# Kernel optimization log

Hardware: AMD Instinct MI355X
Metric: run time of the kernel (lower is better)

The kernel has to match this reference:

```python
import jax, jax.numpy as jnp
import numpy as np

# dims: N sentences, L tokens each, M=2 memory slots/sentence, D hidden, H heads
N, L, M, D, H, FF, V, P, LAYERS = 4, 256, 2, 768, 12, 3072, 32000, 1024, 4
DH = D // H


def setup_inputs() -> dict:
    key = jax.random.key(0)
    ks = jax.random.split(key, 20)
    s = 0.02
    inp = {
        'input_ids': jax.random.randint(ks[0], (N, L), 0, V),
        'memory': jax.random.normal(ks[1], (N, M, D), jnp.float32),
        'emb_table': jax.random.normal(ks[2], (V, D), jnp.float32) * s,
        'pos_table': jax.random.normal(ks[3], (P + 2, D), jnp.float32) * s,
        'Wq': jax.random.normal(ks[4], (LAYERS, D, D), jnp.float32) * s,
        'bq': jnp.zeros((LAYERS, D), jnp.float32),
        'Wk': jax.random.normal(ks[5], (LAYERS, D, D), jnp.float32) * s,
        'bk': jnp.zeros((LAYERS, D), jnp.float32),
        'Wv': jax.random.normal(ks[6], (LAYERS, D, D), jnp.float32) * s,
        'bv': jnp.zeros((LAYERS, D), jnp.float32),
        'W1': jax.random.normal(ks[7], (LAYERS, D, FF), jnp.float32) * s,
        'b1': jnp.zeros((LAYERS, FF), jnp.float32),
        'W2': jax.random.normal(ks[8], (LAYERS, FF, D), jnp.float32) * s,
        'b2': jnp.zeros((LAYERS, D), jnp.float32),
        'g1': jnp.ones((LAYERS, D), jnp.float32),
        'be1': jnp.zeros((LAYERS, D), jnp.float32),
        'g2': jnp.ones((LAYERS, D), jnp.float32),
        'be2': jnp.zeros((LAYERS, D), jnp.float32),
    }
    return inp


def _layer_norm(x, g, b):
    mu = jnp.mean(x, axis=-1, keepdims=True)
    var = jnp.mean((x - mu) ** 2, axis=-1, keepdims=True)
    return (x - mu) / jnp.sqrt(var + 1e-5) * g + b


def _encoder(input_ids, memory, emb_table, pos_table, Wq, bq, Wk, bk, Wv, bv,
             W1, b1, W2, b2, g1, be1, g2, be2):
    base = N * M            # token rows start here in the packed input
    T = base + N * L        # total rows (memory rows + token rows)
    Kk = M + L              # keys per query (own memory + own tokens)

    # position embeddings: memory rows get pos (p % M); tokens get id_pos + M
    mem_pos = jnp.tile(jnp.arange(M), N)                    # (N*M,)
    mem = memory.reshape(N * M, D) + pos_table[mem_pos]
    fwd_pos = jnp.tile(jnp.arange(L) + M, N)                # (N*L,)
    tok = emb_table[input_ids.reshape(-1)] + pos_table[fwd_pos]
    x = jnp.concatenate([mem, tok], axis=0)                 # (T, D)

    # per-sentence key set: its M memory rows then its L token rows
    key_pos = jnp.concatenate([
        jnp.arange(N)[:, None] * M + jnp.arange(M)[None, :],
        base + jnp.arange(N)[:, None] * L + jnp.arange(L)[None, :],
    ], axis=1)                                              # (N, Kk)
    sent = jnp.concatenate([jnp.repeat(jnp.arange(N), M),
                            jnp.repeat(jnp.arange(N), L)])  # (T,)
    gidx = key_pos[sent]                                    # (T, Kk)
    # equal-length sentences => the additive mask built by the torch code is
    # all zeros (key_len == max_key_len for every row), so it is omitted.

    scale = 1.0 / np.sqrt(DH)
    for i in range(LAYERS):
        # K/V are linear row-wise, so project once on all rows then gather
        # (identical math to projecting the gathered tgt, without T-fold GEMM)
        q = (x @ Wq[i] + bq[i]).reshape(T, H, DH)
        kf = (x @ Wk[i] + bk[i]).reshape(T, H, DH)
        vf = (x @ Wv[i] + bv[i]).reshape(T, H, DH)
        kg = kf[gidx]                                       # (T, Kk, H, DH)
        vg = vf[gidx]
        scores = jnp.einsum('thd,tkhd->thk', q, kg) * scale
        probs = jax.nn.softmax(scores, axis=-1)
        ctx = jnp.einsum('thk,tkhd->thd', probs, vg).reshape(T, D)
        x = _layer_norm(x + ctx, g1[i], be1[i])
        h = jax.nn.gelu(x @ W1[i] + b1[i], approximate=False)
        x = _layer_norm(x + h @ W2[i] + b2[i], g2[i], be2[i])

    ret = key_pos[:, M:]                                    # (N, L) token rows
    return x[ret]                                           # (N, L, D)


def reference(input_ids, memory, emb_table, pos_table, Wq, bq, Wk, bk, Wv, bv,
              W1, b1, W2, b2, g1, be1, g2, be2):
    return _encoder(input_ids, memory, emb_table, pos_table, Wq, bq, Wk, bk,
                    Wv, bv, W1, b1, W2, b2, g1, be1, g2, be2)
```

## Files before the change

### kernel.cpp

```cpp
#include <hip/hip_runtime.h>
#include <hip/hip_bf16.h>
#include <math.h>

#define N_      4
#define L_      256
#define M_      2
#define D_      768
#define H_      12
#define FF_     3072
#define DH_     64
#define LAYERS_ 4
#define BASE_   8
#define T_      1032
#define TP_     1088
#define KK_     258
#define QS_     2304
#define PS_     264

typedef __bf16 bf16x8 __attribute__((ext_vector_type(8)));
typedef float  f32x4  __attribute__((ext_vector_type(4)));

__device__ __forceinline__ void async_load16(const __hip_bfloat16* g, __hip_bfloat16* l) {
  __builtin_amdgcn_global_load_lds(
      (const __attribute__((address_space(1))) unsigned int*)g,
      (__attribute__((address_space(3))) unsigned int*)l, 16, 0, 0);
}

__global__ __launch_bounds__(256) void transpose_cast_kernel(
    const float* __restrict__ src, __hip_bfloat16* __restrict__ dst, int K, int N) {
  __shared__ float tile[32][33];
  const int k0 = blockIdx.y * 32, n0 = blockIdx.x * 32;
  const int r = threadIdx.x >> 5, c = threadIdx.x & 31;
  #pragma unroll
  for (int i = 0; i < 4; ++i)
    tile[r + i * 8][c] = src[(size_t)(k0 + r + i * 8) * N + n0 + c];
  __syncthreads();
  #pragma unroll
  for (int i = 0; i < 4; ++i)
    dst[(size_t)(n0 + r + i * 8) * K + k0 + c] = __float2bfloat16(tile[c][r + i * 8]);
}

__global__ __launch_bounds__(256) void pack_bias_kernel(
    const float* __restrict__ bq, const float* __restrict__ bk,
    const float* __restrict__ bv, float* __restrict__ out) {
  int i = blockIdx.x * 256 + threadIdx.x;
  int l = i / QS_, j = i - l * QS_;
  float v;
  if (j < D_)            v = bq[l * D_ + j];
  else if (j < 2 * D_)   v = bk[l * D_ + (j - D_)];
  else                   v = bv[l * D_ + (j - 2 * D_)];
  out[i] = v;
}

__global__ __launch_bounds__(256) void embed_kernel(
    const int* __restrict__ ids, const float* __restrict__ memory,
    const float* __restrict__ emb, const float* __restrict__ pos,
    float* __restrict__ x, __hip_bfloat16* __restrict__ xb) {
  int row = blockIdx.x;
  const float *src, *p;
  if (row < BASE_) {
    src = memory + (long long)row * D_;
    p   = pos + (row & 1) * D_;
  } else {
    int i = row - BASE_;
    int tok = ids[i];
    src = emb + (long long)tok * D_;
    p   = pos + (M_ + (i & (L_ - 1))) * D_;
  }
  for (int d = threadIdx.x; d < D_; d += 256) {
    float v = src[d] + p[d];
    x[(long long)row * D_ + d]  = v;
    xb[(long long)row * D_ + d] = __float2bfloat16(v);
  }
}

template <int ACT, int WF32, int WBF16, int WVT>
__global__ __launch_bounds__(256) void gemm_mfma(
    const __hip_bfloat16* __restrict__ A,
    const __hip_bfloat16* __restrict__ Bt,
    const float* __restrict__ bias,
    float* __restrict__ C,
    __hip_bfloat16* __restrict__ Cb,
    __hip_bfloat16* __restrict__ vt,
    int N, int K) {
  __shared__ __align__(16) __hip_bfloat16 As[4][64][32];
  __shared__ __align__(16) __hip_bfloat16 Bs[4][64][32];
  const int tid  = threadIdx.x;
  const int lane = tid & 63, wid = tid >> 6;
  const int ln   = lane & 15, qd = lane >> 4;
  const int wm   = wid >> 1, wn = wid & 1;

  const size_t arow = (size_t)(blockIdx.y * 64 + wid * 16 + (lane >> 2)) * K + (lane & 3) * 8;
  const size_t brow = (size_t)(blockIdx.x * 64 + wid * 16 + (lane >> 2)) * K + (lane & 3) * 8;

  f32x4 acc[2][2] = {};
  for (int k0 = 0; k0 < K; k0 += 128) {
    #pragma unroll
    for (int s = 0; s < 4; ++s) {
      async_load16(A  + arow + k0 + s * 32, &As[s][wid * 16][0]);
      async_load16(Bt + brow + k0 + s * 32, &Bs[s][wid * 16][0]);
    }
    __syncthreads();
    #pragma unroll
    for (int s = 0; s < 4; ++s) {
      bf16x8 a0 = *(const bf16x8*)&As[s][wm * 32 + ln][qd * 8];
      bf16x8 a1 = *(const bf16x8*)&As[s][wm * 32 + 16 + ln][qd * 8];
      bf16x8 b0 = *(const bf16x8*)&Bs[s][wn * 32 + ln][qd * 8];
      bf16x8 b1 = *(const bf16x8*)&Bs[s][wn * 32 + 16 + ln][qd * 8];
      acc[0][0] = __builtin_amdgcn_mfma_f32_16x16x32_bf16(a0, b0, acc[0][0], 0, 0, 0);
      acc[0][1] = __builtin_amdgcn_mfma_f32_16x16x32_bf16(a0, b1, acc[0][1], 0, 0, 0);
      acc[1][0] = __builtin_amdgcn_mfma_f32_16x16x32_bf16(a1, b0, acc[1][0], 0, 0, 0);
      acc[1][1] = __builtin_amdgcn_mfma_f32_16x16x32_bf16(a1, b1, acc[1][1], 0, 0, 0);
    }
    __syncthreads();
  }
  #pragma unroll
  for (int mt = 0; mt < 2; ++mt) {
    #pragma unroll
    for (int nt = 0; nt < 2; ++nt) {
      const int col = blockIdx.x * 64 + wn * 32 + nt * 16 + ln;
      const float bv = bias[col];
      #pragma unroll
      for (int i = 0; i < 4; ++i) {
        const int row = blockIdx.y * 64 + wm * 32 + mt * 16 + qd * 4 + i;
        float v = acc[mt][nt][i] + bv;
        if (ACT) v = 0.5f * v * (1.f + erff(v * 0.70710678118654752f));
        if (WF32)  C[(size_t)row * N + col]  = v;
        if (WVT) {
          if (col < 2 * D_) Cb[(size_t)row * N + col] = __float2bfloat16(v);
          else              vt[(size_t)(col - 2 * D_) * TP_ + row] = __float2bfloat16(v);
        } else if (WBF16) {
          Cb[(size_t)row * N + col] = __float2bfloat16(v);
        }
      }
    }
  }
}

__global__ __launch_bounds__(256) void attn_mfma(
    const __hip_bfloat16* __restrict__ qkv,
    const __hip_bfloat16* __restrict__ vtb,
    float* __restrict__ ctx) {
  __shared__ __align__(16) __hip_bfloat16 Ps[64][PS_];
  const int qt = blockIdx.x, h = blockIdx.y, b = blockIdx.z;
  const int tid = threadIdx.x;
  const int w = tid >> 6, lane = tid & 63, ln = lane & 15, qd = lane >> 4;

  bf16x8 aq0, aq1;
  {
    int j = qt * 64 + w * 16 + ln;
    int tok = (j < 256) ? (BASE_ + b * L_ + j)
            : ((j < KK_) ? (b * M_ + (j - 256)) : (b * M_));
    const __hip_bfloat16* qp = qkv + (size_t)tok * QS_ + h * DH_ + qd * 8;
    aq0 = *(const bf16x8*)qp;
    aq1 = *(const bf16x8*)(qp + 32);
  }

  f32x4 sa[17];
  #pragma unroll
  for (int nt = 0; nt < 17; ++nt) sa[nt] = (f32x4){0.f, 0.f, 0.f, 0.f};
  #pragma unroll
  for (int nt = 0; nt < 17; ++nt) {
    int key = nt * 16 + ln;
    int ktok = (key < 256) ? (BASE_ + b * L_ + key)
             : ((key < KK_) ? (b * M_ + (key - 256)) : (b * M_));
    const __hip_bfloat16* kp = qkv + (size_t)ktok * QS_ + D_ + h * DH_ + qd * 8;
    bf16x8 b0 = *(const bf16x8*)kp;
    bf16x8 b1 = *(const bf16x8*)(kp + 32);
    sa[nt] = __builtin_amdgcn_mfma_f32_16x16x32_bf16(aq0, b0, sa[nt], 0, 0, 0);
    sa[nt] = __builtin_amdgcn_mfma_f32_16x16x32_bf16(aq1, b1, sa[nt], 0, 0, 0);
  }

  #pragma unroll
  for (int i = 0; i < 4; ++i) {
    float v[17];
    #pragma unroll
    for (int nt = 0; nt < 17; ++nt) v[nt] = sa[nt][i] * 0.125f;
    float mx = -1e30f;
    #pragma unroll
    for (int nt = 0; nt < 16; ++nt) mx = fmaxf(mx, v[nt]);
    if (ln < 2) mx = fmaxf(mx, v[16]);
    #pragma unroll
    for (int m = 1; m < 16; m <<= 1) mx = fmaxf(mx, __shfl_xor(mx, m));
    float sum = 0.f;
    #pragma unroll
    for (int nt = 0; nt < 17; ++nt) {
      float e = (nt == 16 && ln >= 2) ? 0.f : __expf(v[nt] - mx);
      v[nt] = e;
      sum += e;
    }
    #pragma unroll
    for (int m = 1; m < 16; m <<= 1) sum += __shfl_xor(sum, m);
    float is = 1.f / sum;
    const int row = w * 16 + qd * 4 + i;
    #pragma unroll
    for (int nt = 0; nt < 17; ++nt)
      if (nt < 16 || ln < 2)
        Ps[row][nt * 16 + ln] = __float2bfloat16(v[nt] * is);
  }

  f32x4 oa[4] = {};
  #pragma unroll
  for (int k0 = 0; k0 < 8; ++k0) {
    bf16x8 ap = *(const bf16x8*)&Ps[w * 16 + ln][k0 * 32 + qd * 8];
    #pragma unroll
    for (int nt = 0; nt < 4; ++nt) {
      const __hip_bfloat16* vp = vtb + (size_t)(h * DH_ + nt * 16 + ln) * TP_
                               + BASE_ + b * L_ + k0 * 32 + qd * 8;
      bf16x8 bv = *(const bf16x8*)vp;
      oa[nt] = __builtin_amdgcn_mfma_f32_16x16x32_bf16(ap, bv, oa[nt], 0, 0, 0);
    }
  }
  {
    float p0[4], p1[4];
    #pragma unroll
    for (int i = 0; i < 4; ++i) {
      p0[i] = __bfloat162float(Ps[w * 16 + qd * 4 + i][256]);
      p1[i] = __bfloat162float(Ps[w * 16 + qd * 4 + i][257]);
    }
    #pragma unroll
    for (int nt = 0; nt < 4; ++nt) {
      const __hip_bfloat16* vp = vtb + (size_t)(h * DH_ + nt * 16 + ln) * TP_ + b * M_;
      float v0 = __bfloat162float(vp[0]);
      float v1 = __bfloat162float(vp[1]);
      #pragma unroll
      for (int i = 0; i < 4; ++i) oa[nt][i] += p0[i] * v0 + p1[i] * v1;
    }
  }

  #pragma unroll
  for (int i = 0; i < 4; ++i) {
    int j = qt * 64 + w * 16 + qd * 4 + i;
    if (j < KK_) {
      int tok = (j < 256) ? (BASE_ + b * L_ + j) : (b * M_ + (j - 256));
      #pragma unroll
      for (int nt = 0; nt < 4; ++nt)
        ctx[(size_t)tok * D_ + h * DH_ + nt * 16 + ln] = oa[nt][i];
    }
  }
}

__global__ __launch_bounds__(256) void add_ln_kernel(
    float* __restrict__ x, const float* __restrict__ delta,
    const float* __restrict__ g, const float* __restrict__ b,
    __hip_bfloat16* __restrict__ xb) {
  __shared__ float sred[4];
  __shared__ float sbc;
  const int t = blockIdx.x, tid = threadIdx.x;
  float y[3];
  float s = 0.f;
  #pragma unroll
  for (int i = 0; i < 3; ++i) {
    int d = tid + i * 256;
    y[i] = x[(long long)t * D_ + d] + delta[(long long)t * D_ + d];
    s += y[i];
  }
  #pragma unroll
  for (int o = 32; o > 0; o >>= 1) s += __shfl_down(s, o);
  if ((tid & 63) == 0) sred[tid >> 6] = s;
  __syncthreads();
  if (tid == 0) sbc = (sred[0] + sred[1] + sred[2] + sred[3]) * (1.f / D_);
  __syncthreads();
  const float mu = sbc;
  __syncthreads();
  float vs = 0.f;
  #pragma unroll
  for (int i = 0; i < 3; ++i) { float d = y[i] - mu; vs += d * d; }
  #pragma unroll
  for (int o = 32; o > 0; o >>= 1) vs += __shfl_down(vs, o);
  if ((tid & 63) == 0) sred[tid >> 6] = vs;
  __syncthreads();
  if (tid == 0) sbc = (sred[0] + sred[1] + sred[2] + sred[3]) * (1.f / D_);
  __syncthreads();
  const float inv = rsqrtf(sbc + 1e-5f);
  #pragma unroll
  for (int i = 0; i < 3; ++i) {
    int d = tid + i * 256;
    float v = (y[i] - mu) * inv * g[d] + b[d];
    x[(long long)t * D_ + d]  = v;
    xb[(long long)t * D_ + d] = __float2bfloat16(v);
  }
}

__global__ __launch_bounds__(256) void out_copy_kernel(
    const float* __restrict__ x, float* __restrict__ out, int n) {
  int i = blockIdx.x * 256 + threadIdx.x;
  if (i < n) out[i] = x[BASE_ * D_ + i];
}

extern "C" void kernel_launch(void* const* d_in, const int* in_sizes, int n_in,
                              void* d_out, int out_size, void* d_ws, size_t ws_size,
                              hipStream_t stream) {
  const int*   ids    = (const int*)  d_in[0];
  const float* memory = (const float*)d_in[1];
  const float* emb    = (const float*)d_in[2];
  const float* pos    = (const float*)d_in[3];
  const float* Wq     = (const float*)d_in[4];
  const float* bq     = (const float*)d_in[5];
  const float* Wk     = (const float*)d_in[6];
  const float* bk     = (const float*)d_in[7];
  const float* Wv     = (const float*)d_in[8];
  const float* bv     = (const float*)d_in[9];
  const float* W1     = (const float*)d_in[10];
  const float* b1     = (const float*)d_in[11];
  const float* W2     = (const float*)d_in[12];
  const float* b2     = (const float*)d_in[13];
  const float* g1     = (const float*)d_in[14];
  const float* be1    = (const float*)d_in[15];
  const float* g2     = (const float*)d_in[16];
  const float* be2    = (const float*)d_in[17];

  char* w = (char*)d_ws;
  float* x    = (float*)w;                      w += (size_t)TP_ * D_ * 4;
  float* cb   = (float*)w;                      w += (size_t)TP_ * D_ * 4;
  float* bqkv = (float*)w;                      w += (size_t)LAYERS_ * QS_ * 4;
  __hip_bfloat16* xb    = (__hip_bfloat16*)w;   w += (size_t)TP_ * D_ * 2;
  __hip_bfloat16* qkvb  = (__hip_bfloat16*)w;   w += (size_t)TP_ * QS_ * 2;
  __hip_bfloat16* vtb   = (__hip_bfloat16*)w;   w += (size_t)D_ * TP_ * 2;
  __hip_bfloat16* hbb   = (__hip_bfloat16*)w;   w += (size_t)TP_ * FF_ * 2;
  __hip_bfloat16* Wqkvt = (__hip_bfloat16*)w;   w += (size_t)LAYERS_ * QS_ * D_ * 2;
  __hip_bfloat16* W1t   = (__hip_bfloat16*)w;   w += (size_t)LAYERS_ * FF_ * D_ * 2;
  __hip_bfloat16* W2t   = (__hip_bfloat16*)w;   w += (size_t)LAYERS_ * D_ * FF_ * 2;

  for (int i = 0; i < LAYERS_; ++i) {
    const size_t wo  = (size_t)i * D_ * D_;
    const size_t wo1 = (size_t)i * D_ * FF_;
    __hip_bfloat16* dqkv = Wqkvt + (size_t)i * QS_ * D_;
    transpose_cast_kernel<<<dim3(D_ / 32, D_ / 32), 256, 0, stream>>>(Wq + wo, dqkv,                       D_, D_);
    transpose_cast_kernel<<<dim3(D_ / 32, D_ / 32), 256, 0, stream>>>(Wk + wo, dqkv + (size_t)D_ * D_,     D_, D_);
    transpose_cast_kernel<<<dim3(D_ / 32, D_ / 32), 256, 0, stream>>>(Wv + wo, dqkv + (size_t)2 * D_ * D_, D_, D_);
    transpose_cast_kernel<<<dim3(FF_ / 32, D_ / 32), 256, 0, stream>>>(W1 + wo1, W1t + (size_t)i * FF_ * D_, D_, FF_);
    transpose_cast_kernel<<<dim3(D_ / 32, FF_ / 32), 256, 0, stream>>>(W2 + wo1, W2t + (size_t)i * D_ * FF_, FF_, D_);
  }
  pack_bias_kernel<<<LAYERS_ * QS_ / 256, 256, 0, stream>>>(bq, bk, bv, bqkv);

  embed_kernel<<<T_, 256, 0, stream>>>(ids, memory, emb, pos, x, xb);

  for (int i = 0; i < LAYERS_; ++i) {
    gemm_mfma<0, 0, 1, 1><<<dim3(QS_ / 64, TP_ / 64), 256, 0, stream>>>(
        xb, Wqkvt + (size_t)i * QS_ * D_, bqkv + i * QS_, nullptr, qkvb, vtb, QS_, D_);
    attn_mfma<<<dim3(5, H_, N_), 256, 0, stream>>>(qkvb, vtb, cb);
    add_ln_kernel<<<T_, 256, 0, stream>>>(x, cb, g1 + i * D_, be1 + i * D_, xb);
    gemm_mfma<1, 0, 1, 0><<<dim3(FF_ / 64, TP_ / 64), 256, 0, stream>>>(
        xb, W1t + (size_t)i * FF_ * D_, b1 + i * FF_, nullptr, hbb, nullptr, FF_, D_);
    gemm_mfma<0, 1, 0, 0><<<dim3(D_ / 64, TP_ / 64), 256, 0, stream>>>(
        hbb, W2t + (size_t)i * D_ * FF_, b2 + i * D_, cb, nullptr, nullptr, D_, FF_);
    add_ln_kernel<<<T_, 256, 0, stream>>>(x, cb, g2 + i * D_, be2 + i * D_, xb);
  }

  out_copy_kernel<<<(out_size + 255) / 256, 256, 0, stream>>>(x, (float*)d_out, out_size);
}
```

Baseline: 601.2 us.

## Use 128x128 MFMA tiles for QKV/FFN1 GEMMs and batch weight-prep kernels

```diff
diff --git a/kernel.cpp b/kernel.cpp
--- a/kernel.cpp
+++ b/kernel.cpp
@@ -12,7 +12,7 @@
 #define LAYERS_ 4
 #define BASE_   8
 #define T_      1032
-#define TP_     1088
+#define TP_     1152
 #define KK_     258
 #define QS_     2304
 #define PS_     264
@@ -26,7 +26,7 @@
       (__attribute__((address_space(3))) unsigned int*)l, 16, 0, 0);
 }
 
-__global__ __launch_bounds__(256) void transpose_cast_kernel(
+__device__ __forceinline__ void tile_transpose(
     const float* __restrict__ src, __hip_bfloat16* __restrict__ dst, int K, int N) {
   __shared__ float tile[32][33];
   const int k0 = blockIdx.y * 32, n0 = blockIdx.x * 32;
@@ -36,8 +36,35 @@
     tile[r + i * 8][c] = src[(size_t)(k0 + r + i * 8) * N + n0 + c];
   __syncthreads();
   #pragma unroll
-  for (int i = 0; i < 4; ++i)
-    dst[(size_t)(n0 + r + i * 8) * K + k0 + c] = __float2bfloat16(tile[c][r + i * 8]);
+  for (int i = 0; i < 2; ++i) {
+    int e = threadIdx.x + i * 256;
+    int n = e >> 4, kp = e & 15;
+    __hip_bfloat162 v;
+    v.x = __float2bfloat16(tile[2 * kp][n]);
+    v.y = __float2bfloat16(tile[2 * kp + 1][n]);
+    *(__hip_bfloat162*)&dst[(size_t)(n0 + n) * K + k0 + 2 * kp] = v;
+  }
+}
+
+__global__ __launch_bounds__(256) void prep_qkv_kernel(
+    const float* __restrict__ Wq, const float* __restrict__ Wk,
+    const float* __restrict__ Wv, __hip_bfloat16* __restrict__ Wqkvt) {
+  const int z = blockIdx.z, layer = z / 3, which = z - layer * 3;
+  const float* src = (which == 0 ? Wq : which == 1 ? Wk : Wv) + (size_t)layer * D_ * D_;
+  __hip_bfloat16* dst = Wqkvt + (size_t)layer * QS_ * D_ + (size_t)which * D_ * D_;
+  tile_transpose(src, dst, D_, D_);
+}
+
+__global__ __launch_bounds__(256) void prep_w1_kernel(
+    const float* __restrict__ W1, __hip_bfloat16* __restrict__ W1t) {
+  const int z = blockIdx.z;
+  tile_transpose(W1 + (size_t)z * D_ * FF_, W1t + (size_t)z * FF_ * D_, D_, FF_);
+}
+
+__global__ __launch_bounds__(256) void prep_w2_kernel(
+    const float* __restrict__ W2, __hip_bfloat16* __restrict__ W2t) {
+  const int z = blockIdx.z;
+  tile_transpose(W2 + (size_t)z * FF_ * D_, W2t + (size_t)z * D_ * FF_, FF_, D_);
 }
 
 __global__ __launch_bounds__(256) void pack_bias_kernel(
@@ -74,14 +101,84 @@
   }
 }
 
-template <int ACT, int WF32, int WBF16, int WVT>
-__global__ __launch_bounds__(256) void gemm_mfma(
+template <int ACT, int WOUT>
+__global__ __launch_bounds__(256) void gemm_mfma128(
     const __hip_bfloat16* __restrict__ A,
     const __hip_bfloat16* __restrict__ Bt,
     const float* __restrict__ bias,
     float* __restrict__ C,
     __hip_bfloat16* __restrict__ Cb,
     __hip_bfloat16* __restrict__ vt,
+    int N, int K) {
+  __shared__ __align__(16) __hip_bfloat16 As[2][128][32];
+  __shared__ __align__(16) __hip_bfloat16 Bs[2][128][32];
+  const int tid  = threadIdx.x;
+  const int lane = tid & 63, wid = tid >> 6;
+  const int ln   = lane & 15, qd = lane >> 4;
+  const int wm   = wid >> 1, wn = wid & 1;
+  const int lr   = lane >> 2;
+  const int lc   = (lane & 3) * 8;
+
+  f32x4 acc[4][4] = {};
+  for (int k0 = 0; k0 < K; k0 += 64) {
+    #pragma unroll
+    for (int s = 0; s < 2; ++s) {
+      #pragma unroll
+      for (int i = 0; i < 2; ++i) {
+        const int rr = wid * 16 + i * 64 + lr;
+        async_load16(A  + (size_t)(blockIdx.y * 128 + rr) * K + k0 + s * 32 + lc,
+                     &As[s][wid * 16 + i * 64][0]);
+        async_load16(Bt + (size_t)(blockIdx.x * 128 + rr) * K + k0 + s * 32 + lc,
+                     &Bs[s][wid * 16 + i * 64][0]);
+      }
+    }
+    __syncthreads();
+    #pragma unroll
+    for (int s = 0; s < 2; ++s) {
+      bf16x8 af[4], bf[4];
+      #pragma unroll
+      for (int t = 0; t < 4; ++t) {
+        af[t] = *(const bf16x8*)&As[s][wm * 64 + t * 16 + ln][qd * 8];
+        bf[t] = *(const bf16x8*)&Bs[s][wn * 64 + t * 16 + ln][qd * 8];
+      }
+      #pragma unroll
+      for (int mt = 0; mt < 4; ++mt)
+        #pragma unroll
+        for (int nt = 0; nt < 4; ++nt)
+          acc[mt][nt] = __builtin_amdgcn_mfma_f32_16x16x32_bf16(af[mt], bf[nt], acc[mt][nt], 0, 0, 0);
+    }
+    __syncthreads();
+  }
+  #pragma unroll
+  for (int mt = 0; mt < 4; ++mt) {
+    #pragma unroll
+    for (int nt = 0; nt < 4; ++nt) {
+      const int col = blockIdx.x * 128 + wn * 64 + nt * 16 + ln;
+      const float bv = bias[col];
+      #pragma unroll
+      for (int i = 0; i < 4; ++i) {
+        const int row = blockIdx.y * 128 + wm * 64 + mt * 16 + qd * 4 + i;
+        float v = acc[mt][nt][i] + bv;
+        if (ACT) v = 0.5f * v * (1.f + erff(v * 0.70710678118654752f));
+        if (WOUT == 1) {
+          C[(size_t)row * N + col] = v;
+        } else if (WOUT == 2) {
+          if (col < 2 * D_) Cb[(size_t)row * N + col] = __float2bfloat16(v);
+          else              vt[(size_t)(col - 2 * D_) * TP_ + row] = __float2bfloat16(v);
+        } else {
+          Cb[(size_t)row * N + col] = __float2bfloat16(v);
+        }
+      }
+    }
+  }
+}
+
+template <int ACT, int WF32>
+__global__ __launch_bounds__(256) void gemm_mfma64(
+    const __hip_bfloat16* __restrict__ A,
+    const __hip_bfloat16* __restrict__ Bt,
+    const float* __restrict__ bias,
+    float* __restrict__ C, __hip_bfloat16* __restrict__ Cb,
     int N, int K) {
   __shared__ __align__(16) __hip_bfloat16 As[4][64][32];
   __shared__ __align__(16) __hip_bfloat16 Bs[4][64][32];
@@ -125,13 +222,8 @@
         const int row = blockIdx.y * 64 + wm * 32 + mt * 16 + qd * 4 + i;
         float v = acc[mt][nt][i] + bv;
         if (ACT) v = 0.5f * v * (1.f + erff(v * 0.70710678118654752f));
-        if (WF32)  C[(size_t)row * N + col]  = v;
-        if (WVT) {
-          if (col < 2 * D_) Cb[(size_t)row * N + col] = __float2bfloat16(v);
-          else              vt[(size_t)(col - 2 * D_) * TP_ + row] = __float2bfloat16(v);
-        } else if (WBF16) {
-          Cb[(size_t)row * N + col] = __float2bfloat16(v);
-        }
+        if (WF32) C[(size_t)row * N + col]  = v;
+        else      Cb[(size_t)row * N + col] = __float2bfloat16(v);
       }
     }
   }
@@ -322,29 +414,22 @@
   __hip_bfloat16* W1t   = (__hip_bfloat16*)w;   w += (size_t)LAYERS_ * FF_ * D_ * 2;
   __hip_bfloat16* W2t   = (__hip_bfloat16*)w;   w += (size_t)LAYERS_ * D_ * FF_ * 2;
 
+  prep_qkv_kernel<<<dim3(D_ / 32, D_ / 32, LAYERS_ * 3), 256, 0, stream>>>(Wq, Wk, Wv, Wqkvt);
+  prep_w1_kernel<<<dim3(FF_ / 32, D_ / 32, LAYERS_), 256, 0, stream>>>(W1, W1t);
+  prep_w2_kernel<<<dim3(D_ / 32, FF_ / 32, LAYERS_), 256, 0, stream>>>(W2, W2t);
+  pack_bias_kernel<<<LAYERS_ * QS_ / 256, 256, 0, stream>>>(bq, bk, bv, bqkv);
+
+  embed_kernel<<<T_, 256, 0, stream>>>(ids, memory, emb, pos, x, xb);
+
   for (int i = 0; i < LAYERS_; ++i) {
-    const size_t wo  = (size_t)i * D_ * D_;
-    const size_t wo1 = (size_t)i * D_ * FF_;
-    __hip_bfloat16* dqkv = Wqkvt + (size_t)i * QS_ * D_;
-    transpose_cast_kernel<<<dim3(D_ / 32, D_ / 32), 256, 0, stream>>>(Wq + wo, dqkv,                       D_, D_);
-    transpose_cast_kernel<<<dim3(D_ / 32, D_ / 32), 256, 0, stream>>>(Wk + wo, dqkv + (size_t)D_ * D_,     D_, D_);
-    transpose_cast_kernel<<<dim3(D_ / 32, D_ / 32), 256, 0, stream>>>(Wv + wo, dqkv + (size_t)2 * D_ * D_, D_, D_);
-    transpose_cast_kernel<<<dim3(FF_ / 32, D_ / 32), 256, 0, stream>>>(W1 + wo1, W1t + (size_t)i * FF_ * D_, D_, FF_);
-    transpose_cast_kernel<<<dim3(D_ / 32, FF_ / 32), 256, 0, stream>>>(W2 + wo1, W2t + (size_t)i * D_ * FF_, FF_, D_);
-  }
-  pack_bias_kernel<<<LAYERS_ * QS_ / 256, 256, 0, stream>>>(bq, bk, bv, bqkv);
-
-  embed_kernel<<<T_, 256, 0, stream>>>(ids, memory, emb, pos, x, xb);
-
-  for (int i = 0; i < LAYERS_; ++i) {
-    gemm_mfma<0, 0, 1, 1><<<dim3(QS_ / 64, TP_ / 64), 256, 0, stream>>>(
+    gemm_mfma128<0, 2><<<dim3(QS_ / 128, TP_ / 128), 256, 0, stream>>>(
         xb, Wqkvt + (size_t)i * QS_ * D_, bqkv + i * QS_, nullptr, qkvb, vtb, QS_, D_);
     attn_mfma<<<dim3(5, H_, N_), 256, 0, stream>>>(qkvb, vtb, cb);
     add_ln_kernel<<<T_, 256, 0, stream>>>(x, cb, g1 + i * D_, be1 + i * D_, xb);
-    gemm_mfma<1, 0, 1, 0><<<dim3(FF_ / 64, TP_ / 64), 256, 0, stream>>>(
+    gemm_mfma128<1, 0><<<dim3(FF_ / 128, TP_ / 128), 256, 0, stream>>>(
         xb, W1t + (size_t)i * FF_ * D_, b1 + i * FF_, nullptr, hbb, nullptr, FF_, D_);
-    gemm_mfma<0, 1, 0, 0><<<dim3(D_ / 64, TP_ / 64), 256, 0, stream>>>(
-        hbb, W2t + (size_t)i * D_ * FF_, b2 + i * D_, cb, nullptr, nullptr, D_, FF_);
+    gemm_mfma64<0, 1><<<dim3(D_ / 64, TP_ / 64), 256, 0, stream>>>(
+        hbb, W2t + (size_t)i * D_ * FF_, b2 + i * D_, cb, nullptr, D_, FF_);
     add_ln_kernel<<<T_, 256, 0, stream>>>(x, cb, g2 + i * D_, be2 + i * D_, xb);
   }
 
```

Result: slower. 643.6 us (+7.1%).
